# Kernel optimization log

Measured on AMD Instinct MI355X. Metric: run time of the kernel, lower is better.

The kernel has to match this reference:

```python
import jax, jax.numpy as jnp
import numpy as np

B, T, D, H = 64, 256, 1024, 1024


def setup_inputs() -> dict:
    key = jax.random.key(0)
    ks = jax.random.split(key, 7)
    s = 0.02
    x = jax.random.normal(ks[0], (B, T, D), dtype=jnp.float32)
    # packed gate weights, gate order [i, f, g, o] along last dim (4H)
    Wx0 = jax.random.normal(ks[1], (D, 4 * H), dtype=jnp.float32) * s
    Wh0 = jax.random.normal(ks[2], (H, 4 * H), dtype=jnp.float32) * s
    b0 = jnp.zeros((4 * H,), dtype=jnp.float32)
    Wx1 = jax.random.normal(ks[3], (H, 4 * H), dtype=jnp.float32) * s
    Wh1 = jax.random.normal(ks[4], (H, 4 * H), dtype=jnp.float32) * s
    b1 = jnp.zeros((4 * H,), dtype=jnp.float32)
    return {"x": x, "Wx0": Wx0, "Wh0": Wh0, "b0": b0, "Wx1": Wx1, "Wh1": Wh1, "b1": b1}


def _cell(h, c, xt, Wx, Wh, b):
    gates = xt @ Wx + h @ Wh + b  # [B, 4H]
    i, f, g, o = jnp.split(gates, 4, axis=-1)
    c_new = jax.nn.sigmoid(f) * c + jax.nn.sigmoid(i) * jnp.tanh(g)
    h_new = jax.nn.sigmoid(o) * jnp.tanh(c_new)
    return h_new, c_new


def reference(x, Wx0, Wh0, b0, Wx1, Wh1, b1):
    b = x.shape[0]
    h = x.dtype
    z = jnp.zeros((b, Wh0.shape[0]), dtype=x.dtype)
    carry0 = (z, z, z, z)  # (h0, c0, h1, c1), zero-initialized like flax initialize_carry

    def step(carry, xt):
        h0, c0, h1, c1 = carry
        h0, c0 = _cell(h0, c0, xt, Wx0, Wh0, b0)
        h1, c1 = _cell(h1, c1, h0, Wx1, Wh1, b1)
        return (h0, c0, h1, c1), None

    xs = jnp.swapaxes(x, 0, 1)  # [T, B, D]
    (h0, c0, h1, c1), _ = jax.lax.scan(step, carry0, xs)
    return h1  # last-timestep output of top layer, [B, H]
```

## Files before the change

kernel.cpp:

```cpp
#include <hip/hip_runtime.h>
#include <cmath>

#define TSTEPS 256
#define DIM 1024

typedef _Float16 half8v __attribute__((ext_vector_type(8)));
typedef _Float16 half4v __attribute__((ext_vector_type(4)));
typedef float f32x4 __attribute__((ext_vector_type(4)));
typedef unsigned long long u64;


__global__ void prologue(const float* __restrict__ x, _Float16* __restrict__ xh,
                         _Float16* __restrict__ hrings, unsigned* __restrict__ cnts)
{
    size_t gid  = (size_t)blockIdx.x * blockDim.x + threadIdx.x;
    size_t nthr = (size_t)gridDim.x * blockDim.x;
    for (size_t i = gid; i < 4194304u; i += nthr) {
        float4 v = ((const float4*)x)[i];
        half4v h = {(_Float16)v.x, (_Float16)v.y, (_Float16)v.z, (_Float16)v.w};
        unsigned d4 = (unsigned)i & 255u, t = ((unsigned)i >> 8) & 255u, b = (unsigned)i >> 16;
        ((half4v*)(xh + ((size_t)t * 64 + b) * 1024))[d4] = h;
    }
    for (size_t i = gid; i < 65536u; i += nthr) {
        half8v z = {};
        ((half8v*)hrings)[i] = z;
    }
    for (size_t i = gid; i < 139264u; i += nthr) cnts[i] = 0u;
}

__global__ __launch_bounds__(512, 2)
void lstm_persistent(const float* __restrict__ Wx0, const float* __restrict__ Wh0,
                     const float* __restrict__ b0,
                     const float* __restrict__ Wx1, const float* __restrict__ Wh1,
                     const float* __restrict__ b1,
                     const _Float16* __restrict__ xh, _Float16* __restrict__ h0r,
                     _Float16* __restrict__ h1r, unsigned* __restrict__ cnts,
                     float* __restrict__ out)
{
    extern __shared__ char smem[];
    _Float16* wfrag = (_Float16*)smem;
    float*    gates = (float*)smem;
    _Float16* hlds  = (_Float16*)(smem + 102400);

    const int tid  = threadIdx.x;
    const int blk  = blockIdx.x;
    const int cell = blk >> 7;
    const int wb   = blk & 127;
    const int lane = tid & 63, kq = tid >> 6;
    const int n15 = lane & 15, q = lane >> 4;

    unsigned* leaf0 = cnts;
    unsigned* leaf1 = cnts + 65536;
    unsigned* leafm = cell ? leaf1 : leaf0;

    const float* m0 = cell ? Wx1 : Wx0;
    const float* m1 = cell ? Wh1 : Wh0;
    for (int idx = tid; idx < 16384; idx += 512) {
        int k = idx >> 3;
        int cc0 = (idx & 7) * 4;
        int g = cc0 >> 3, c = cc0 & 7;
        const float* src = (k < 1024 ? m0 + (size_t)k * 4096
                                     : m1 + (size_t)(k - 1024) * 4096)
                           + g * 1024 + wb * 8 + c;
        float4 v = *(const float4*)src;
        int skq = k >> 8, kt = (k >> 5) & 7, sq = (k >> 3) & 3, j = k & 7;
        float vv[4] = {v.x, v.y, v.z, v.w};
        #pragma unroll
        for (int e = 0; e < 4; ++e) {
            int cc = cc0 + e, nt = cc >> 4, nn = cc & 15;
            wfrag[((((skq * 2 + nt) * 8 + kt) * 64) + sq * 16 + nn) * 8 + j] = (_Float16)vv[e];
        }
    }
    __syncthreads();

    half8v wreg[16];
    #pragma unroll
    for (int nt = 0; nt < 2; ++nt)
        #pragma unroll
        for (int kt = 0; kt < 8; ++kt)
            wreg[nt * 8 + kt] = *(const half8v*)
                &wfrag[((((kq * 2 + nt) * 8 + kt) * 64) + lane) * 8];
    __syncthreads();

    const int pb = tid >> 3, pd = tid & 7;
    const float* bias = cell ? b1 : b0;
    const int gdim = wb * 8 + pd;
    const float bi = bias[0 * 1024 + gdim], bfg = bias[1 * 1024 + gdim],
                bg = bias[2 * 1024 + gdim], bo  = bias[3 * 1024 + gdim];
    float creg = 0.0f;

    const bool havex = (cell == 0) && (kq < 4);
    const int  xw    = (n15 & 7) << 2;
    const int  xrr   = (pd & 7) << 2;

    for (int p = 0; p <= TSTEPS; ++p) {
        if (cell == 0 && p == TSTEPS) break;
        const bool active = cell ? (p >= 1) : true;

        half8v A[4][8];
        if (havex) {
            const _Float16* a = xh + (size_t)p * 65536 + (size_t)n15 * 1024
                                + kq * 256 + q * 8;
            #pragma unroll
            for (int mt = 0; mt < 4; ++mt)
                #pragma unroll
                for (int kt = 0; kt < 8; ++kt)
                    A[mt][kt] = *(const half8v*)(a + mt * 16384 + kt * 32);
        }

        if (tid < 64) {
            if (p >= 1) {
                const unsigned* addr = nullptr;
                if (tid < 16) {
                    addr = leaf0 + ((p - 1) * 16 + tid) * 16;
                } else if (tid < 32) {
                    int lf = tid - 16;
                    if (cell == 0) { if (p >= 3) addr = leaf1 + ((p - 3) * 16 + lf) * 16; }
                    else           { if (p >= 2) addr = leaf1 + ((p - 1) * 16 + lf) * 16; }
                }
                bool ok = (addr == nullptr);
                while (true) {
                    if (!ok)
                        ok = __hip_atomic_load(addr, __ATOMIC_RELAXED,
                                               __HIP_MEMORY_SCOPE_AGENT) >= 8u;
                    if (__ballot(ok) == ~0ull) break;
                    __builtin_amdgcn_s_sleep(4);
                }
            }
            __builtin_amdgcn_fence(__ATOMIC_ACQUIRE, "agent");
        }
        __syncthreads();

        if (active && !havex) {
            const _Float16* hb;
            int wq;
            if (cell == 0)      { hb = h0r + (size_t)((p - 1) & 3) * 65536; wq = (kq - 4) * 32; }
            else if (kq < 4)    { hb = h0r + (size_t)((p - 1) & 3) * 65536; wq = kq * 32; }
            else                { hb = h1r + (size_t)((p - 2) & 3) * 65536; wq = (kq - 4) * 32; }
            const _Float16* a = hb + (size_t)(wq + q) * 512 + (size_t)n15 * 8;
            #pragma unroll
            for (int mt = 0; mt < 4; ++mt)
                #pragma unroll
                for (int kt = 0; kt < 8; ++kt)
                    A[mt][kt] = *(const half8v*)(a + kt * 2048 + mt * 128);
        }

        if (active) {
            #pragma unroll
            for (int mt = 0; mt < 4; ++mt) {
                f32x4 acc0 = {0.f, 0.f, 0.f, 0.f};
                f32x4 acc1 = {0.f, 0.f, 0.f, 0.f};
                #pragma unroll
                for (int kt = 0; kt < 8; ++kt) {
                    acc0 = __builtin_amdgcn_mfma_f32_16x16x32_f16(A[mt][kt], wreg[kt],     acc0, 0, 0, 0);
                    acc1 = __builtin_amdgcn_mfma_f32_16x16x32_f16(A[mt][kt], wreg[8 + kt], acc1, 0, 0, 0);
                }
                const int row0 = mt * 16 + q * 4;
                *(f32x4*)(gates + ((((n15      * 8 + kq) * 64) + row0) ^ xw)) = acc0;
                *(f32x4*)(gates + (((((16+n15) * 8 + kq) * 64) + row0) ^ xw)) = acc1;
            }
        }
        __syncthreads();

        if (active) {
            float gg[4];
            #pragma unroll
            for (int g = 0; g < 4; ++g) {
                const int c = g * 8 + pd;
                float s = 0.f;
                #pragma unroll
                for (int k8 = 0; k8 < 8; ++k8)
                    s += gates[(((c * 8 + k8) * 64) + pb) ^ xrr];
                gg[g] = s;
            }
            float g0 = gg[0] + bi, g1 = gg[1] + bfg, g2 = gg[2] + bg, g3 = gg[3] + bo;
            float si = 1.f / (1.f + __expf(-g0));
            float sf = 1.f / (1.f + __expf(-g1));
            float so = 1.f / (1.f + __expf(-g3));
            float tg = 1.f - 2.f / (__expf(2.f * g2) + 1.f);
            float cn = sf * creg + si * tg;
            float tc = 1.f - 2.f / (__expf(2.f * cn) + 1.f);
            float hn = so * tc;
            creg = cn;
            hlds[pb * 8 + pd] = (_Float16)hn;
            if (cell && p == TSTEPS) out[pb * 1024 + gdim] = hn;
        }

        if (p < TSTEPS) {
            if (active) __syncthreads();
            if (tid < 64) {
                if (active) {
                    const u64* hp = (const u64*)(hlds + tid * 8);
                    u64 lo = hp[0], hi = hp[1];
                    _Float16* dst = (cell ? h1r + (size_t)((p - 1) & 3) * 65536
                                          : h0r + (size_t)(p & 3) * 65536)
                                    + (size_t)wb * 512;
                    u64* dp = (u64*)dst + tid * 2;
                    __hip_atomic_store(dp,     lo, __ATOMIC_RELAXED, __HIP_MEMORY_SCOPE_AGENT);
                    __hip_atomic_store(dp + 1, hi, __ATOMIC_RELAXED, __HIP_MEMORY_SCOPE_AGENT);
                    asm volatile("s_waitcnt vmcnt(0)" ::: "memory");
                }
                if (tid == 0)
                    __hip_atomic_fetch_add(leafm + (p * 16 + (wb >> 3)) * 16, 1u,
                                           __ATOMIC_RELAXED, __HIP_MEMORY_SCOPE_AGENT);
            }
        }
    }
}

extern "C" void kernel_launch(void* const* d_in, const int* in_sizes, int n_in,
                              void* d_out, int out_size, void* d_ws, size_t ws_size,
                              hipStream_t stream)
{
    const float* x   = (const float*)d_in[0];
    const float* Wx0 = (const float*)d_in[1];
    const float* Wh0 = (const float*)d_in[2];
    const float* b0  = (const float*)d_in[3];
    const float* Wx1 = (const float*)d_in[4];
    const float* Wh1 = (const float*)d_in[5];
    const float* b1  = (const float*)d_in[6];
    float* out = (float*)d_out;

    _Float16* xh   = (_Float16*)d_ws;
    _Float16* h0r  = xh + (size_t)16777216;
    _Float16* h1r  = h0r + 262144;
    unsigned* cnts = (unsigned*)(h1r + 262144);

    hipLaunchKernelGGL(prologue, dim3(2048), dim3(256), 0, stream, x, xh, h0r, cnts);

    size_t smem = 131072;
    (void)hipFuncSetAttribute((const void*)lstm_persistent,
                              hipFuncAttributeMaxDynamicSharedMemorySize, (int)smem);

    void* args[] = {(void*)&Wx0, (void*)&Wh0, (void*)&b0,
                    (void*)&Wx1, (void*)&Wh1, (void*)&b1,
                    (void*)&xh, (void*)&h0r, (void*)&h1r,
                    (void*)&cnts, (void*)&out};
    (void)hipLaunchCooperativeKernel((const void*)lstm_persistent, dim3(256), dim3(512),
                                     args, (unsigned)smem, stream);
}
```

Measured before the change: 2.312 ms.

## Retile persistent LSTM blocks as 32 batch rows by 16 hidden dims

Each workgroup previously owned 8 hidden dims across all 64 batch rows. It now owns 16 hidden dims (64 gate columns) for half the batch, split by mb/nb. Each wave holds 32 weight fragments in registers over a quarter of K and loads half as many activation rows. The goal is to halve the activation bytes each block reads per timestep and to give each A fragment more MFMAs. In exchange, weight register pressure doubles, the weight preload runs in two passes, and the h ring layout and the gates LDS swizzle change.

```diff
diff --git a/kernel.cpp b/kernel.cpp
--- a/kernel.cpp
+++ b/kernel.cpp
@@ -40,12 +40,13 @@
     extern __shared__ char smem[];
     _Float16* wfrag = (_Float16*)smem;
     float*    gates = (float*)smem;
-    _Float16* hlds  = (_Float16*)(smem + 102400);
+    _Float16* hlds  = (_Float16*)(smem + 65536);
 
     const int tid  = threadIdx.x;
     const int blk  = blockIdx.x;
     const int cell = blk >> 7;
     const int wb   = blk & 127;
+    const int mb   = wb >> 6, nb = wb & 63;
     const int lane = tid & 63, kq = tid >> 6;
     const int n15 = lane & 15, q = lane >> 4;
 
@@ -53,56 +54,59 @@
     unsigned* leaf1 = cnts + 65536;
     unsigned* leafm = cell ? leaf1 : leaf0;
 
-    const float* m0 = cell ? Wx1 : Wx0;
-    const float* m1 = cell ? Wh1 : Wh0;
-    for (int idx = tid; idx < 16384; idx += 512) {
-        int k = idx >> 3;
-        int cc0 = (idx & 7) * 4;
-        int g = cc0 >> 3, c = cc0 & 7;
-        const float* src = (k < 1024 ? m0 + (size_t)k * 4096
-                                     : m1 + (size_t)(k - 1024) * 4096)
-                           + g * 1024 + wb * 8 + c;
-        float4 v = *(const float4*)src;
-        int skq = k >> 8, kt = (k >> 5) & 7, sq = (k >> 3) & 3, j = k & 7;
-        float vv[4] = {v.x, v.y, v.z, v.w};
-        #pragma unroll
-        for (int e = 0; e < 4; ++e) {
-            int cc = cc0 + e, nt = cc >> 4, nn = cc & 15;
-            wfrag[((((skq * 2 + nt) * 8 + kt) * 64) + sq * 16 + nn) * 8 + j] = (_Float16)vv[e];
-        }
-    }
-    __syncthreads();
-
-    half8v wreg[16];
-    #pragma unroll
-    for (int nt = 0; nt < 2; ++nt)
-        #pragma unroll
-        for (int kt = 0; kt < 8; ++kt)
-            wreg[nt * 8 + kt] = *(const half8v*)
-                &wfrag[((((kq * 2 + nt) * 8 + kt) * 64) + lane) * 8];
-    __syncthreads();
-
-    const int pb = tid >> 3, pd = tid & 7;
+    half8v wreg[32];
+    {
+        const float* passW[2] = { cell ? Wx1 : Wx0, cell ? Wh1 : Wh0 };
+        for (int ps = 0; ps < 2; ++ps) {
+            const float* W = passW[ps];
+            for (int idx = tid; idx < 16384; idx += 512) {
+                int k = idx >> 4;
+                int cc0 = (idx & 15) * 4;
+                const float* src = W + (size_t)k * 4096
+                                   + (cc0 >> 4) * 1024 + nb * 16 + (cc0 & 15);
+                float4 v = *(const float4*)src;
+                int skq = k >> 8, kt = (k >> 5) & 7, qp = (k >> 3) & 3, j = k & 7;
+                float vv[4] = {v.x, v.y, v.z, v.w};
+                #pragma unroll
+                for (int e = 0; e < 4; ++e) {
+                    int cc = cc0 + e, nt = cc >> 4, nn = cc & 15;
+                    wfrag[((((skq * 4 + nt) * 8 + kt) * 64) + qp * 16 + nn) * 8 + j]
+                        = (_Float16)vv[e];
+                }
+            }
+            __syncthreads();
+            if ((kq >> 2) == ps) {
+                int skq = kq & 3;
+                #pragma unroll
+                for (int nt = 0; nt < 4; ++nt)
+                    #pragma unroll
+                    for (int kt = 0; kt < 8; ++kt)
+                        wreg[nt * 8 + kt] = *(const half8v*)
+                            &wfrag[((((skq * 4 + nt) * 8 + kt) * 64) + lane) * 8];
+            }
+            __syncthreads();
+        }
+    }
+
+    const int pm = tid >> 4, pdn = tid & 15;
     const float* bias = cell ? b1 : b0;
-    const int gdim = wb * 8 + pd;
-    const float bi = bias[0 * 1024 + gdim], bfg = bias[1 * 1024 + gdim],
-                bg = bias[2 * 1024 + gdim], bo  = bias[3 * 1024 + gdim];
+    const int dimg = nb * 16 + pdn;
+    const float bi = bias[0 * 1024 + dimg], bfg = bias[1 * 1024 + dimg],
+                bg = bias[2 * 1024 + dimg], bo  = bias[3 * 1024 + dimg];
     float creg = 0.0f;
 
     const bool havex = (cell == 0) && (kq < 4);
-    const int  xw    = (n15 & 7) << 2;
-    const int  xrr   = (pd & 7) << 2;
 
     for (int p = 0; p <= TSTEPS; ++p) {
         if (cell == 0 && p == TSTEPS) break;
         const bool active = cell ? (p >= 1) : true;
 
-        half8v A[4][8];
+        half8v A[2][8];
         if (havex) {
-            const _Float16* a = xh + (size_t)p * 65536 + (size_t)n15 * 1024
-                                + kq * 256 + q * 8;
-            #pragma unroll
-            for (int mt = 0; mt < 4; ++mt)
+            const _Float16* a = xh + (size_t)p * 65536
+                                + (size_t)(mb * 32 + n15) * 1024 + kq * 256 + q * 8;
+            #pragma unroll
+            for (int mt = 0; mt < 2; ++mt)
                 #pragma unroll
                 for (int kt = 0; kt < 8; ++kt)
                     A[mt][kt] = *(const half8v*)(a + mt * 16384 + kt * 32);
@@ -132,32 +136,38 @@
         __syncthreads();
 
         if (active && !havex) {
-            const _Float16* hb;
-            int wq;
-            if (cell == 0)      { hb = h0r + (size_t)((p - 1) & 3) * 65536; wq = (kq - 4) * 32; }
-            else if (kq < 4)    { hb = h0r + (size_t)((p - 1) & 3) * 65536; wq = kq * 32; }
-            else                { hb = h1r + (size_t)((p - 2) & 3) * 65536; wq = (kq - 4) * 32; }
-            const _Float16* a = hb + (size_t)(wq + q) * 512 + (size_t)n15 * 8;
-            #pragma unroll
-            for (int mt = 0; mt < 4; ++mt)
+            const _Float16* hb; int ks;
+            if (cell == 0)   { hb = h0r + (size_t)((p - 1) & 3) * 65536; ks = kq - 4; }
+            else if (kq < 4) { hb = h0r + (size_t)((p - 1) & 3) * 65536; ks = kq; }
+            else             { hb = h1r + (size_t)((p - 2) & 3) * 65536; ks = kq - 4; }
+            const _Float16* a = hb + (size_t)mb * 32768
+                                + (size_t)(ks * 16 + (q >> 1)) * 512
+                                + (size_t)n15 * 16 + (q & 1) * 8;
+            #pragma unroll
+            for (int mt = 0; mt < 2; ++mt)
                 #pragma unroll
                 for (int kt = 0; kt < 8; ++kt)
-                    A[mt][kt] = *(const half8v*)(a + kt * 2048 + mt * 128);
+                    A[mt][kt] = *(const half8v*)(a + kt * 1024 + mt * 256);
         }
 
         if (active) {
             #pragma unroll
-            for (int mt = 0; mt < 4; ++mt) {
-                f32x4 acc0 = {0.f, 0.f, 0.f, 0.f};
-                f32x4 acc1 = {0.f, 0.f, 0.f, 0.f};
-                #pragma unroll
-                for (int kt = 0; kt < 8; ++kt) {
-                    acc0 = __builtin_amdgcn_mfma_f32_16x16x32_f16(A[mt][kt], wreg[kt],     acc0, 0, 0, 0);
-                    acc1 = __builtin_amdgcn_mfma_f32_16x16x32_f16(A[mt][kt], wreg[8 + kt], acc1, 0, 0, 0);
-                }
+            for (int mt = 0; mt < 2; ++mt) {
+                f32x4 acc[4] = {{0.f,0.f,0.f,0.f}, {0.f,0.f,0.f,0.f},
+                                {0.f,0.f,0.f,0.f}, {0.f,0.f,0.f,0.f}};
+                #pragma unroll
+                for (int kt = 0; kt < 8; ++kt)
+                    #pragma unroll
+                    for (int nt = 0; nt < 4; ++nt)
+                        acc[nt] = __builtin_amdgcn_mfma_f32_16x16x32_f16(
+                                      A[mt][kt], wreg[nt * 8 + kt], acc[nt], 0, 0, 0);
                 const int row0 = mt * 16 + q * 4;
-                *(f32x4*)(gates + ((((n15      * 8 + kq) * 64) + row0) ^ xw)) = acc0;
-                *(f32x4*)(gates + (((((16+n15) * 8 + kq) * 64) + row0) ^ xw)) = acc1;
+                #pragma unroll
+                for (int nt = 0; nt < 4; ++nt) {
+                    const int c = nt * 16 + n15;
+                    *(f32x4*)(gates + (c * 8 + kq) * 32
+                                    + (row0 ^ ((c & 7) << 2))) = acc[nt];
+                }
             }
         }
         __syncthreads();
@@ -166,11 +176,12 @@
             float gg[4];
             #pragma unroll
             for (int g = 0; g < 4; ++g) {
-                const int c = g * 8 + pd;
+                const int c = g * 16 + pdn;
+                const int key = (c & 7) << 2;
                 float s = 0.f;
                 #pragma unroll
                 for (int k8 = 0; k8 < 8; ++k8)
-                    s += gates[(((c * 8 + k8) * 64) + pb) ^ xrr];
+                    s += gates[(c * 8 + k8) * 32 + (pm ^ key)];
                 gg[g] = s;
             }
             float g0 = gg[0] + bi, g1 = gg[1] + bfg, g2 = gg[2] + bg, g3 = gg[3] + bo;
@@ -182,8 +193,8 @@
             float tc = 1.f - 2.f / (__expf(2.f * cn) + 1.f);
             float hn = so * tc;
             creg = cn;
-            hlds[pb * 8 + pd] = (_Float16)hn;
-            if (cell && p == TSTEPS) out[pb * 1024 + gdim] = hn;
+            hlds[tid] = (_Float16)hn;
+            if (cell && p == TSTEPS) out[(mb * 32 + pm) * 1024 + nb * 16 + pdn] = hn;
         }
 
         if (p < TSTEPS) {
@@ -194,7 +205,7 @@
                     u64 lo = hp[0], hi = hp[1];
                     _Float16* dst = (cell ? h1r + (size_t)((p - 1) & 3) * 65536
                                           : h0r + (size_t)(p & 3) * 65536)
-                                    + (size_t)wb * 512;
+                                    + (size_t)mb * 32768 + (size_t)nb * 512;
                     u64* dp = (u64*)dst + tid * 2;
                     __hip_atomic_store(dp,     lo, __ATOMIC_RELAXED, __HIP_MEMORY_SCOPE_AGENT);
                     __hip_atomic_store(dp + 1, hi, __ATOMIC_RELAXED, __HIP_MEMORY_SCOPE_AGENT);
```

New measurement: 2.057 ms. 11.0% less time.
